# Performance work log

Measured on AMD Instinct MI355X. Metric: run time of the kernel, lower is better.

Reference implementation:

```python
import jax, jax.numpy as jnp
import numpy as np

B, T, C = 4, 1024, 512
H, HD = 8, 64
NE, K = 8, 2
FF = 4 * C


def setup_inputs() -> dict:
    key = jax.random.key(0)
    ks = jax.random.split(key, 16)
    s = 0.02
    return {
        "x": jax.random.normal(ks[0], (B, T, C), jnp.float32),
        "ln1_g": jnp.ones((C,), jnp.float32),
        "ln1_b": jnp.zeros((C,), jnp.float32),
        "ln2_g": jnp.ones((C,), jnp.float32),
        "ln2_b": jnp.zeros((C,), jnp.float32),
        "Wq": jax.random.normal(ks[1], (H, C, HD), jnp.float32) * s,
        "Wk": jax.random.normal(ks[2], (H, C, HD), jnp.float32) * s,
        "Wv": jax.random.normal(ks[3], (H, C, HD), jnp.float32) * s,
        "Wp": jax.random.normal(ks[4], (H * HD, C), jnp.float32) * s,
        "bp": jnp.zeros((C,), jnp.float32),
        "Wr": jax.random.normal(ks[5], (C, NE), jnp.float32) * s,
        "br": jnp.zeros((NE,), jnp.float32),
        "W1": jax.random.normal(ks[6], (NE, C, FF), jnp.float32) * s,
        "b1": jnp.zeros((NE, FF), jnp.float32),
        "W2": jax.random.normal(ks[7], (NE, FF, C), jnp.float32) * s,
        "b2": jnp.zeros((NE, C), jnp.float32),
    }


def _ln(x, g, b, eps=1e-5):
    mu = jnp.mean(x, axis=-1, keepdims=True)
    var = jnp.var(x, axis=-1, keepdims=True)
    return (x - mu) * jax.lax.rsqrt(var + eps) * g + b


def reference(x, ln1_g, ln1_b, ln2_g, ln2_b, Wq, Wk, Wv, Wp, bp, Wr, br, W1, b1, W2, b2):
    # --- multi-head causal attention (all heads stacked) ---
    h = _ln(x, ln1_g, ln1_b)
    q = jnp.einsum("btc,hcd->bhtd", h, Wq)
    k = jnp.einsum("btc,hcd->bhtd", h, Wk)
    v = jnp.einsum("btc,hcd->bhtd", h, Wv)
    wei = jnp.einsum("bhtd,bhsd->bhts", q, k) / np.sqrt(HD).astype(np.float32)
    causal = jnp.tril(jnp.ones((T, T), bool))
    wei = jnp.where(causal, wei, -jnp.inf)
    wei = jax.nn.softmax(wei, axis=-1)
    attn = jnp.einsum("bhts,bhsd->bhtd", wei, v)  # [B,H,T,HD]
    attn = attn.transpose(0, 2, 1, 3).reshape(B, T, H * HD)
    x2 = x + attn @ Wp + bp

    # --- SparseMoE: dense all-experts compute, masked top-k combine ---
    h2 = _ln(x2, ln2_g, ln2_b)
    scores = h2 @ Wr + br  # [B,T,NE]
    topk_scores, indices = jax.lax.top_k(scores, K)
    # scatter top-k scores into zeros (rest stays 0), then softmax over experts
    mask = jnp.sum(jax.nn.one_hot(indices, NE, dtype=scores.dtype) * topk_scores[..., None], axis=-2)
    router = jax.nn.softmax(mask, axis=-1)  # [B,T,NE]
    hid = jax.nn.relu(jnp.einsum("btc,ecf->btef", h2, W1) + b1)  # [B,T,NE,FF]
    eo = jnp.einsum("btef,efc->btec", hid, W2) + b2  # [B,T,NE,C]
    moe = jnp.einsum("bte,btec->btc", router, eo)
    return x2 + moe
```

## Files before the change

kernel.cpp:

```cpp
#include <hip/hip_runtime.h>


typedef unsigned short u16;
typedef __attribute__((ext_vector_type(8))) short s16x8;
typedef __attribute__((ext_vector_type(4))) float f32x4;

__device__ __forceinline__ u16 f2bf(float f) {
  union { float f; unsigned u; } v; v.f = f;
  unsigned r = v.u + 0x7fffu + ((v.u >> 16) & 1u);
  return (u16)(r >> 16);
}
__device__ __forceinline__ float bf2f(u16 h) {
  union { unsigned u; float f; } v; v.u = ((unsigned)h) << 16;
  return v.f;
}

#define GLDS16(g, s) __builtin_amdgcn_global_load_lds( \
    (const __attribute__((address_space(1))) void*)(g), \
    (__attribute__((address_space(3))) void*)(s), 16, 0, 0)

#define MFMA16(a, b, c) __builtin_amdgcn_mfma_f32_16x16x32_bf16((a), (b), (c), 0, 0, 0)

__global__ __launch_bounds__(256) void transpose_k(
    const float* __restrict__ in, u16* __restrict__ out,
    int R, int C, long long ibs, long long obs, float scale)
{
  __shared__ float tile[32][33];
  in  += (long long)blockIdx.z * ibs;
  out += (long long)blockIdx.z * obs;
  const int c0 = blockIdx.x * 32, r0 = blockIdx.y * 32;
  const int tx = threadIdx.x, ty = threadIdx.y;
  #pragma unroll
  for (int i = 0; i < 4; ++i)
    tile[ty + i*8][tx] = in[(size_t)(r0 + ty + i*8) * C + c0 + tx];
  __syncthreads();
  #pragma unroll
  for (int i = 0; i < 4; ++i)
    out[(size_t)(c0 + ty + i*8) * R + r0 + tx] = f2bf(tile[tx][ty + i*8] * scale);
}

__global__ __launch_bounds__(256) void transqkv_k(
    const float* __restrict__ Wq, const float* __restrict__ Wk,
    const float* __restrict__ Wv, u16* __restrict__ out)
{
  __shared__ float tile[32][33];
  const int z = blockIdx.z, which = z >> 3, head = z & 7;
  const float* in = (which == 0 ? Wq : (which == 1 ? Wk : Wv)) + (size_t)head * 512 * 64;
  u16* o = out + (size_t)which * 512 * 512 + (size_t)head * 64 * 512;
  const float scale = (which == 0) ? 0.125f : 1.f;
  const int c0 = blockIdx.x * 32, r0 = blockIdx.y * 32;
  const int tx = threadIdx.x, ty = threadIdx.y;
  #pragma unroll
  for (int i = 0; i < 4; ++i)
    tile[ty + i*8][tx] = in[(size_t)(r0 + ty + i*8) * 64 + c0 + tx];
  __syncthreads();
  #pragma unroll
  for (int i = 0; i < 4; ++i)
    o[(size_t)(c0 + ty + i*8) * 512 + r0 + tx] = f2bf(tile[tx][ty + i*8] * scale);
}

__global__ __launch_bounds__(256) void vtrans_k(
    const u16* __restrict__ qkv, u16* __restrict__ vt)
{
  __shared__ u16 tile[32][33];
  const int bh = blockIdx.z, b = bh >> 3, h = bh & 7;
  const int t0 = blockIdx.x * 32, d0 = blockIdx.y * 32;
  const int tx = threadIdx.x, ty = threadIdx.y;
  #pragma unroll
  for (int i = 0; i < 4; ++i)
    tile[ty + i*8][tx] = qkv[(size_t)(b*1024 + t0 + ty + i*8) * 1536 + 1024 + h*64 + d0 + tx];
  __syncthreads();
  #pragma unroll
  for (int i = 0; i < 4; ++i)
    vt[(size_t)bh*65536 + (size_t)(d0 + ty + i*8) * 1024 + t0 + tx] = tile[tx][ty + i*8];
}

__global__ __launch_bounds__(256) void ln_k(
    const float* __restrict__ x, const float* __restrict__ g,
    const float* __restrict__ b, u16* __restrict__ o)
{
  const int row = blockIdx.x, t = threadIdx.x;
  const float* xr = x + (size_t)row * 512;
  const float a0 = xr[t], a1 = xr[t + 256];
  float s = a0 + a1, ss = a0*a0 + a1*a1;
  #pragma unroll
  for (int off = 1; off < 64; off <<= 1) {
    s  += __shfl_xor(s, off);
    ss += __shfl_xor(ss, off);
  }
  __shared__ float rs[4], rq[4];
  const int w = t >> 6;
  if ((t & 63) == 0) { rs[w] = s; rq[w] = ss; }
  __syncthreads();
  s  = rs[0] + rs[1] + rs[2] + rs[3];
  ss = rq[0] + rq[1] + rq[2] + rq[3];
  const float mu = s * (1.f/512.f);
  const float var = ss * (1.f/512.f) - mu*mu;
  const float rstd = rsqrtf(var + 1e-5f);
  o[(size_t)row*512 + t]       = f2bf((a0 - mu) * rstd * g[t]     + b[t]);
  o[(size_t)row*512 + t + 256] = f2bf((a1 - mu) * rstd * g[t+256] + b[t+256]);
}

template<int BN, int EPI>
__global__ __launch_bounds__(256) void gemm2p(
    const u16* __restrict__ A, const u16* __restrict__ Bt,
    int M, int N, int K, int lda, int ldb,
    u16* __restrict__ obf, float* __restrict__ oa,
    const float* __restrict__ bias, const float* __restrict__ extra, int e0)
{
  constexpr int NB = BN / 32;
  constexpr int SB = BN / 32;
  __shared__ u16 Asm[2][128*64];
  __shared__ u16 Bsm[2][BN*64];
  const int t = threadIdx.x, l = t & 63;
  const int wid = t >> 6, wr = wid >> 1, wc = wid & 1;
  const int lrow = l & 15, lhi = l >> 4;
  const int m0 = blockIdx.x * 128, n0 = blockIdx.y * BN;

  const f32x4 z4 = {0.f, 0.f, 0.f, 0.f};
  f32x4 acc[4][NB];
  #pragma unroll
  for (int i = 0; i < 4; ++i)
    #pragma unroll
    for (int j = 0; j < NB; ++j) acc[i][j] = z4;

  const u16* ga = A  + (size_t)(m0 + (t >> 3)) * lda + (t & 7) * 8;
  const u16* gb = Bt + (size_t)(n0 + (t >> 3)) * ldb + (t & 7) * 8;

#define STG2(buf, k0) do { \
    _Pragma("unroll") \
    for (int i = 0; i < 4; ++i) \
      GLDS16(ga + (size_t)(i*32)*lda + (k0), (char*)Asm[buf] + i*4096 + t*16); \
    _Pragma("unroll") \
    for (int i = 0; i < SB; ++i) \
      GLDS16(gb + (size_t)(i*32)*ldb + (k0), (char*)Bsm[buf] + i*4096 + t*16); \
  } while (0)

  const int NT = K >> 6;
  STG2(0, 0);
  for (int tt = 0; tt < NT; ++tt) {
    if (tt + 1 < NT) {
      STG2((tt + 1) & 1, (tt + 1) * 64);
      if constexpr (BN == 128) asm volatile("s_waitcnt vmcnt(8)" ::: "memory");
      else                     asm volatile("s_waitcnt vmcnt(6)" ::: "memory");
    } else {
      asm volatile("s_waitcnt vmcnt(0)" ::: "memory");
    }
    __builtin_amdgcn_sched_barrier(0);
    __builtin_amdgcn_s_barrier();
    const u16* As = Asm[tt & 1];
    const u16* Bs = Bsm[tt & 1];
    #pragma unroll
    for (int kh = 0; kh < 2; ++kh) {
      s16x8 af[4], bfr[NB];
      #pragma unroll
      for (int i = 0; i < 4; ++i)
        af[i]  = *(const s16x8*)(As + (wr*64 + i*16 + lrow)*64 + kh*32 + lhi*8);
      #pragma unroll
      for (int j = 0; j < NB; ++j)
        bfr[j] = *(const s16x8*)(Bs + (wc*(BN/2) + j*16 + lrow)*64 + kh*32 + lhi*8);
      #pragma unroll
      for (int i = 0; i < 4; ++i)
        #pragma unroll
        for (int j = 0; j < NB; ++j)
          acc[i][j] = MFMA16(af[i], bfr[j], acc[i][j]);
    }
    __builtin_amdgcn_s_barrier();
    __builtin_amdgcn_sched_barrier(0);
  }
#undef STG2

  #pragma unroll
  for (int i = 0; i < 4; ++i) {
    const int rbase = m0 + wr*64 + i*16 + lhi*4;
    #pragma unroll
    for (int j = 0; j < NB; ++j) {
      const int col = n0 + wc*(BN/2) + j*16 + lrow;
      #pragma unroll
      for (int rr = 0; rr < 4; ++rr) {
        const int row = rbase + rr;
        const float v = acc[i][j][rr];
        if (EPI == 0) {
          obf[(size_t)row*N + col] = f2bf(v);
        } else if (EPI == 1) {
          const float r = extra[(size_t)row*8 + e0 + (col >> 11)];
          obf[(size_t)row*N + col] = f2bf(fmaxf(v + bias[col], 0.f) * r);
        } else {
          oa[(size_t)row*N + col] = v + bias[col] + extra[(size_t)row*N + col];
        }
      }
    }
  }
}

template<int NKT, int EPI>
__global__ __launch_bounds__(512, 2) void gemm8p(
    const u16* __restrict__ A, const u16* __restrict__ Bt,
    int lda, int ldb,
    u16* __restrict__ obf,
    const float* __restrict__ bias, const float* __restrict__ rout)
{
  __shared__ u16 Lds[2][2][256*64];
  const int t = threadIdx.x, l = t & 63;
  const int wid = t >> 6, wm = wid >> 2, wn = wid & 3;
  const int lrow = l & 15, lhi = l >> 4;

  int m0, n0, zz = 0;
  {
    const int bid = blockIdx.x;
    const int r = bid & 7, k = bid >> 3;
    if (EPI == 1) { m0 = (k >> 3) * 256; n0 = (r * 8 + (k & 7)) * 256; }
    else { zz = r + (k >> 3) * 8; m0 = ((k & 7) >> 1) * 256; n0 = (k & 1) * 256; }
  }
  const u16* Ab = A  + (size_t)m0 * lda + (EPI == 4 ? zz * 512 : 0);
  const u16* Bb = Bt + (size_t)n0 * ldb + (EPI == 4 ? zz * 512 : 0);

  const int tr = t >> 3;
  const int sc = ((t & 7) ^ (tr & 7)) * 8;

#define STG(bf, kt, hx) do { \
    const int X_ = (hx) >> 1, h_ = (hx) & 1; \
    const u16* s_ = X_ ? Bb : Ab; \
    const int ld_ = X_ ? ldb : lda; \
    char* d_ = (char*)&Lds[bf][X_][0] + h_*16384 + t*16; \
    GLDS16(s_ + (size_t)(h_*128 + tr) * ld_ + (kt)*64 + sc, d_); \
    GLDS16(s_ + (size_t)(h_*128 + 64 + tr) * ld_ + (kt)*64 + sc, d_ + 8192); \
  } while (0)

#define RD(Ls, row, kb) (*(const s16x8*)((const char*)(Ls) + (row)*128 + ((kb) ^ (((row)&7)<<4))))

  f32x4 acc[8][4];
  const f32x4 z4 = {0.f, 0.f, 0.f, 0.f};
  #pragma unroll
  for (int i = 0; i < 8; ++i)
    #pragma unroll
    for (int j = 0; j < 4; ++j) acc[i][j] = z4;

  #pragma unroll
  for (int kt = 0; kt < 2; ++kt)
    #pragma unroll
    for (int hx = 0; hx < 4; ++hx) STG(kt & 1, kt, hx);
  asm volatile("s_waitcnt vmcnt(8)" ::: "memory");
  __builtin_amdgcn_sched_barrier(0);
  __builtin_amdgcn_s_barrier();

  s16x8 frA[2][4], frB[2][2];
  #pragma unroll
  for (int X = 0; X < NKT; ++X) {
    const u16* As = &Lds[X & 1][0][0];
    const u16* Bs = &Lds[X & 1][1][0];
    #pragma unroll
    for (int q = 0; q < 4; ++q) {
      const int mh = q >> 1, nh = q & 1;
      if (nh == 0) {
        #pragma unroll
        for (int kk = 0; kk < 2; ++kk)
          #pragma unroll
          for (int mf = 0; mf < 4; ++mf) {
            const int row = wm*128 + (mh*4 + mf)*16 + lrow;
            frA[kk][mf] = RD(As, row, kk*64 + lhi*16);
          }
      }
      #pragma unroll
      for (int kk = 0; kk < 2; ++kk)
        #pragma unroll
        for (int nf = 0; nf < 2; ++nf) {
          const int row = wn*64 + (nh*2 + nf)*16 + lrow;
          frB[kk][nf] = RD(Bs, row, kk*64 + lhi*16);
        }
      {
        const int P = 4*X + q;
        if (P >= 3) {
          const int kts = ((P - 3) >> 2) + 2, hh = (P - 3) & 3;
          if (kts < NKT) STG(kts & 1, kts, hh);
        }
      }
      __builtin_amdgcn_s_barrier();
      asm volatile("s_waitcnt lgkmcnt(0)" ::: "memory");
      __builtin_amdgcn_sched_barrier(0);
      __builtin_amdgcn_s_setprio(1);
      #pragma unroll
      for (int kk = 0; kk < 2; ++kk)
        #pragma unroll
        for (int mf = 0; mf < 4; ++mf)
          #pragma unroll
          for (int nf = 0; nf < 2; ++nf)
            acc[mh*4 + mf][nh*2 + nf] =
                MFMA16(frA[kk][mf], frB[kk][nf], acc[mh*4 + mf][nh*2 + nf]);
      __builtin_amdgcn_s_setprio(0);
      if (q == 3 && X + 1 < NKT) {
        if (X + 2 < NKT) asm volatile("s_waitcnt vmcnt(2)" ::: "memory");
        else             asm volatile("s_waitcnt vmcnt(0)" ::: "memory");
        __builtin_amdgcn_sched_barrier(0);
      }
      __builtin_amdgcn_s_barrier();
    }
  }
#undef STG
#undef RD

  u16* outp = (EPI == 4) ? obf + (size_t)zz * 1024 * 512 : obf;
  #pragma unroll
  for (int mf = 0; mf < 8; ++mf) {
    const int rbase = m0 + wm*128 + mf*16 + lhi*4;
    #pragma unroll
    for (int nf = 0; nf < 4; ++nf) {
      const int col = n0 + wn*64 + nf*16 + lrow;
      #pragma unroll
      for (int rr = 0; rr < 4; ++rr) {
        const int row = rbase + rr;
        const float v = acc[mf][nf][rr];
        if (EPI == 1) {
          const float r = rout[(size_t)row*8 + (col >> 11)];
          outp[(size_t)row*16384 + col] = f2bf(fmaxf(v + bias[col], 0.f) * r);
        } else {
          outp[(size_t)row*512 + col] = f2bf(v);
        }
      }
    }
  }
}

__global__ __launch_bounds__(256) void combineQ_k(
    float* __restrict__ outq, const u16* __restrict__ P,
    const float* __restrict__ routq, const float* __restrict__ b2)
{
  const int row = blockIdx.x, t = threadIdx.x;
  const int c = t * 2;
  float r[8];
  #pragma unroll
  for (int e = 0; e < 8; ++e) r[e] = routq[(size_t)row*8 + e];
  float v0 = outq[(size_t)row*512 + c];
  float v1 = outq[(size_t)row*512 + c + 1];
  #pragma unroll
  for (int z = 0; z < 32; ++z) {
    const unsigned pv = *(const unsigned*)(P + (size_t)z*524288 + (size_t)row*512 + c);
    v0 += bf2f((u16)(pv & 0xffffu));
    v1 += bf2f((u16)(pv >> 16));
  }
  #pragma unroll
  for (int e = 0; e < 8; ++e) {
    v0 += r[e] * b2[(size_t)e*512 + c];
    v1 += r[e] * b2[(size_t)e*512 + c + 1];
  }
  outq[(size_t)row*512 + c]     = v0;
  outq[(size_t)row*512 + c + 1] = v1;
}

__global__ __launch_bounds__(256) void gemm2_k(
    const u16* __restrict__ hid, const u16* __restrict__ w2t,
    u16* __restrict__ P, int e0, int accum)
{
  __shared__ u16 Asm[128*64];
  __shared__ u16 Bsm[64*64];
  const int t = threadIdx.x;
  const int l = t & 63;
  const int wid = t >> 6, wr = wid >> 1, wc = wid & 1;
  const int lrow = l & 15, lhi = l >> 4;
  const int m0 = blockIdx.x * 128, n0 = blockIdx.y * 64, z = blockIdx.z;

  const u16* A  = hid + z * 2048;
  const u16* Bt = w2t + (size_t)(e0 + z) * 512 * 2048;
  u16* Pz = P + (size_t)z * 4096 * 512;

  const f32x4 z4 = {0.f, 0.f, 0.f, 0.f};
  f32x4 acc[4][2];
  #pragma unroll
  for (int i = 0; i < 4; ++i) { acc[i][0] = z4; acc[i][1] = z4; }

  const u16* ga = A  + (size_t)(m0 + (t >> 3)) * 4096 + (t & 7) * 8;
  const u16* gb = Bt + (size_t)(n0 + (t >> 3)) * 2048 + (t & 7) * 8;

  for (int k0 = 0; k0 < 2048; k0 += 64) {
    #pragma unroll
    for (int i = 0; i < 4; ++i)
      GLDS16(ga + (size_t)i*32*4096 + k0, (char*)Asm + i*4096 + t*16);
    #pragma unroll
    for (int i = 0; i < 2; ++i)
      GLDS16(gb + (size_t)i*32*2048 + k0, (char*)Bsm + i*4096 + t*16);
    __syncthreads();
    #pragma unroll
    for (int kh = 0; kh < 2; ++kh) {
      s16x8 af[4], bfr[2];
      #pragma unroll
      for (int i = 0; i < 4; ++i)
        af[i]  = *(const s16x8*)(Asm + (wr*64 + i*16 + lrow)*64 + kh*32 + lhi*8);
      #pragma unroll
      for (int j = 0; j < 2; ++j)
        bfr[j] = *(const s16x8*)(Bsm + (wc*32 + j*16 + lrow)*64 + kh*32 + lhi*8);
      #pragma unroll
      for (int i = 0; i < 4; ++i)
        #pragma unroll
        for (int j = 0; j < 2; ++j)
          acc[i][j] = MFMA16(af[i], bfr[j], acc[i][j]);
    }
    __syncthreads();
  }

  #pragma unroll
  for (int i = 0; i < 4; ++i) {
    const int rbase = m0 + wr*64 + i*16 + lhi*4;
    #pragma unroll
    for (int j = 0; j < 2; ++j) {
      const int col = n0 + wc*32 + j*16 + lrow;
      #pragma unroll
      for (int rr = 0; rr < 4; ++rr) {
        const size_t idx = (size_t)(rbase + rr) * 512 + col;
        const float old = accum ? bf2f(Pz[idx]) : 0.f;
        Pz[idx] = f2bf(old + acc[i][j][rr]);
      }
    }
  }
}

__global__ __launch_bounds__(256) void combineB_k(
    float* __restrict__ out, const u16* __restrict__ P,
    const float* __restrict__ rout, const float* __restrict__ b2)
{
  const int row = blockIdx.x, t = threadIdx.x;
  float r[8];
  #pragma unroll
  for (int e = 0; e < 8; ++e) r[e] = rout[(size_t)row*8 + e];
  #pragma unroll
  for (int cc = 0; cc < 2; ++cc) {
    const int c = t + cc*256;
    const size_t idx = (size_t)row*512 + c;
    float v = out[idx] + bf2f(P[idx]) + bf2f(P[(size_t)4096*512 + idx]);
    #pragma unroll
    for (int e = 0; e < 8; ++e) v += r[e] * b2[(size_t)e*512 + c];
    out[idx] = v;
  }
}

__global__ __launch_bounds__(256) void attn_k(
    const u16* __restrict__ qkv, const u16* __restrict__ vt, u16* __restrict__ o)
{
  const int bid = blockIdx.x;
  const int xcd = bid & 7, rr_ = bid >> 3;
  const int bh = (rr_ >> 4) * 8 + xcd;
  const int qb = rr_ & 15;
  const int b = bh >> 3, h = bh & 7;
  const int t = threadIdx.x, l = t & 63, w = t >> 6;
  const int lrow = l & 15, lhi = l >> 4;
  const int t0w = qb*64 + w*16;

  __shared__ u16 Ksm[2][64*64];
  __shared__ u16 Vsm[2][64*64];
  __shared__ u16 Psm[4][16][72];

  const u16* qrow = qkv + (size_t)(b*1024 + t0w + lrow) * 1536 + h*64 + lhi*8;
  s16x8 qf0 = *(const s16x8*)qrow;
  s16x8 qf1 = *(const s16x8*)(qrow + 32);

  const f32x4 z4 = {0.f,0.f,0.f,0.f};
  float m[4], sl[4];
  f32x4 oacc[4];
  #pragma unroll
  for (int i = 0; i < 4; ++i) { m[i] = -1e30f; sl[i] = 0.f; oacc[i] = z4; }

  const int trow = t >> 3;
  const int csw = ((t & 7) ^ (trow & 7)) * 8;
  const u16* gk = qkv + (size_t)(b*1024 + trow) * 1536 + 512 + h*64 + csw;
  const u16* gv = vt + (size_t)bh*65536 + (size_t)trow*1024 + csw;
  const int nt = qb + 1;

#define ASTAGE(buf, s0) do { \
    _Pragma("unroll") \
    for (int i = 0; i < 2; ++i) { \
      GLDS16(gk + (size_t)((s0) + i*32) * 1536, (char*)Ksm[buf] + i*4096 + t*16); \
      GLDS16(gv + (s0) + (size_t)(i*32)*1024,   (char*)Vsm[buf] + i*4096 + t*16); \
    } } while (0)

  ASTAGE(0, 0);
  for (int kv = 0; kv < nt; ++kv) {
    const int s0 = kv * 64;
    if (kv + 1 < nt) {
      ASTAGE((kv + 1) & 1, s0 + 64);
      asm volatile("s_waitcnt vmcnt(4)" ::: "memory");
    } else {
      asm volatile("s_waitcnt vmcnt(0)" ::: "memory");
    }
    __builtin_amdgcn_s_barrier();
    __builtin_amdgcn_sched_barrier(0);
    const u16* Ks = Ksm[kv & 1];
    const u16* Vs = Vsm[kv & 1];

    f32x4 sacc[4] = {z4, z4, z4, z4};
    #pragma unroll
    for (int n = 0; n < 4; ++n) {
      const int r = n*16 + lrow;
      s16x8 kf0 = *(const s16x8*)((const char*)Ks + r*128 + ((lhi*16) ^ ((r & 7) << 4)));
      s16x8 kf1 = *(const s16x8*)((const char*)Ks + r*128 + ((64 + lhi*16) ^ ((r & 7) << 4)));
      sacc[n] = MFMA16(qf0, kf0, sacc[n]);
      sacc[n] = MFMA16(qf1, kf1, sacc[n]);
    }
    if (s0 + 63 > t0w) {
      #pragma unroll
      for (int n = 0; n < 4; ++n)
        #pragma unroll
        for (int rr = 0; rr < 4; ++rr)
          if (s0 + n*16 + lrow > t0w + lhi*4 + rr) sacc[n][rr] = -1e30f;
    }
    float pm[4];
    #pragma unroll
    for (int rr = 0; rr < 4; ++rr)
      pm[rr] = fmaxf(fmaxf(sacc[0][rr], sacc[1][rr]), fmaxf(sacc[2][rr], sacc[3][rr]));
    #pragma unroll
    for (int rr = 0; rr < 4; ++rr) {
      pm[rr] = fmaxf(pm[rr], __shfl_xor(pm[rr], 1));
      pm[rr] = fmaxf(pm[rr], __shfl_xor(pm[rr], 2));
      pm[rr] = fmaxf(pm[rr], __shfl_xor(pm[rr], 4));
      pm[rr] = fmaxf(pm[rr], __shfl_xor(pm[rr], 8));
    }
    float p[4][4], ps[4], scv[4];
    #pragma unroll
    for (int rr = 0; rr < 4; ++rr) {
      const float mn = fmaxf(m[rr], pm[rr]);
      scv[rr] = __expf(m[rr] - mn);
      m[rr] = mn;
      ps[rr] = 0.f;
      #pragma unroll
      for (int n = 0; n < 4; ++n) {
        p[n][rr] = __expf(sacc[n][rr] - mn);
        ps[rr] += p[n][rr];
      }
    }
    #pragma unroll
    for (int rr = 0; rr < 4; ++rr) {
      ps[rr] += __shfl_xor(ps[rr], 1);
      ps[rr] += __shfl_xor(ps[rr], 2);
      ps[rr] += __shfl_xor(ps[rr], 4);
      ps[rr] += __shfl_xor(ps[rr], 8);
      sl[rr] = sl[rr] * scv[rr] + ps[rr];
    }
    #pragma unroll
    for (int ct = 0; ct < 4; ++ct) {
      f32x4 t4 = oacc[ct];
      #pragma unroll
      for (int rr = 0; rr < 4; ++rr) t4[rr] *= scv[rr];
      oacc[ct] = t4;
    }
    #pragma unroll
    for (int n = 0; n < 4; ++n)
      #pragma unroll
      for (int rr = 0; rr < 4; ++rr)
        Psm[w][lhi*4 + rr][n*16 + lrow] = f2bf(p[n][rr]);
    asm volatile("s_waitcnt lgkmcnt(0)" ::: "memory");
    __builtin_amdgcn_sched_barrier(0);
    s16x8 pa0 = *(const s16x8*)&Psm[w][lrow][lhi*8];
    s16x8 pa1 = *(const s16x8*)&Psm[w][lrow][32 + lhi*8];
    #pragma unroll
    for (int ct = 0; ct < 4; ++ct) {
      const int r = ct*16 + lrow;
      s16x8 vb0 = *(const s16x8*)((const char*)Vs + r*128 + ((lhi*16) ^ ((r & 7) << 4)));
      s16x8 vb1 = *(const s16x8*)((const char*)Vs + r*128 + ((64 + lhi*16) ^ ((r & 7) << 4)));
      oacc[ct] = MFMA16(pa0, vb0, oacc[ct]);
      oacc[ct] = MFMA16(pa1, vb1, oacc[ct]);
    }
    __builtin_amdgcn_s_barrier();
    __builtin_amdgcn_sched_barrier(0);
  }
#undef ASTAGE
  #pragma unroll
  for (int ct = 0; ct < 4; ++ct)
    #pragma unroll
    for (int rr = 0; rr < 4; ++rr) {
      const int row = b*1024 + t0w + lhi*4 + rr;
      o[(size_t)row*512 + h*64 + ct*16 + lrow] = f2bf(oacc[ct][rr] / sl[rr]);
    }
}

__global__ __launch_bounds__(256) void router_k(
    const float* __restrict__ x2, const float* __restrict__ g,
    const float* __restrict__ b, const float* __restrict__ Wr,
    const float* __restrict__ br, float* __restrict__ rt,
    u16* __restrict__ h2o)
{
  const int l = threadIdx.x & 63, w = threadIdx.x >> 6;
  const int tkn = blockIdx.x * 4 + w;
  const float* xr = x2 + (size_t)tkn * 512;
  float v[8];
  float s = 0.f, ss = 0.f;
  #pragma unroll
  for (int i = 0; i < 8; ++i) {
    v[i] = xr[l*8 + i];
    s += v[i]; ss += v[i]*v[i];
  }
  #pragma unroll
  for (int off = 1; off < 64; off <<= 1) {
    s  += __shfl_xor(s, off);
    ss += __shfl_xor(ss, off);
  }
  const float mu = s * (1.f/512.f);
  const float var = ss * (1.f/512.f) - mu*mu;
  const float rstd = rsqrtf(var + 1e-5f);
  float acc[8];
  #pragma unroll
  for (int e = 0; e < 8; ++e) acc[e] = 0.f;
  s16x8 hw;
  #pragma unroll
  for (int i = 0; i < 8; ++i) {
    const int c = l*8 + i;
    const float hv = (v[i] - mu) * rstd * g[c] + b[c];
    hw[i] = (short)f2bf(hv);
    const float* wrow = Wr + (size_t)c * 8;
    #pragma unroll
    for (int e = 0; e < 8; ++e) acc[e] += hv * wrow[e];
  }
  *(s16x8*)(h2o + (size_t)tkn*512 + l*8) = hw;
  #pragma unroll
  for (int e = 0; e < 8; ++e) {
    #pragma unroll
    for (int off = 1; off < 64; off <<= 1) acc[e] += __shfl_xor(acc[e], off);
    acc[e] += br[e];
  }
  int e1 = 0;
  #pragma unroll
  for (int e = 1; e < 8; ++e) if (acc[e] > acc[e1]) e1 = e;
  int e2 = (e1 == 0) ? 1 : 0;
  #pragma unroll
  for (int e = 0; e < 8; ++e) if (e != e1 && acc[e] > acc[e2]) e2 = e;
  const float mx = fmaxf(acc[e1], 0.f);
  float Z = 0.f;
  #pragma unroll
  for (int e = 0; e < 8; ++e) {
    const float mv = (e == e1 || e == e2) ? acc[e] : 0.f;
    Z += __expf(mv - mx);
  }
  if (l < 8) {
    const float mv = (l == e1 || l == e2) ? acc[l] : 0.f;
    rt[(size_t)tkn * 8 + l] = __expf(mv - mx) / Z;
  }
}

extern "C" void kernel_launch(void* const* d_in, const int* in_sizes, int n_in,
                              void* d_out, int out_size, void* d_ws, size_t ws_size,
                              hipStream_t stream) {
  const float* x    = (const float*)d_in[0];
  const float* ln1g = (const float*)d_in[1];
  const float* ln1b = (const float*)d_in[2];
  const float* ln2g = (const float*)d_in[3];
  const float* ln2b = (const float*)d_in[4];
  const float* Wq   = (const float*)d_in[5];
  const float* Wk   = (const float*)d_in[6];
  const float* Wv   = (const float*)d_in[7];
  const float* Wp   = (const float*)d_in[8];
  const float* bp   = (const float*)d_in[9];
  const float* Wr   = (const float*)d_in[10];
  const float* br   = (const float*)d_in[11];
  const float* W1   = (const float*)d_in[12];
  const float* b1   = (const float*)d_in[13];
  const float* W2   = (const float*)d_in[14];
  const float* b2   = (const float*)d_in[15];
  float* out = (float*)d_out;

  const int pathN = (ws_size >= (size_t)104988672) ? 1 : 0;

  char* ws = (char*)d_ws;
  size_t off = 0;
  auto alloc = [&](size_t bytes) -> char* {
    char* p = ws + off;
    off += (bytes + 255) & ~(size_t)255;
    return p;
  };
  u16* w1_t = (u16*)alloc((size_t)8*2048*512*2);
  u16* w2f  = (u16*)alloc((size_t)8*512*2048*2);
  u16* h2b  = (u16*)alloc((size_t)4096*512*2);
  float* rout = (float*)alloc((size_t)4096*8*4);
  u16* hidq = (u16*)alloc((size_t)4096*4096*2);
  u16* Ppl  = (u16*)alloc(pathN ? (size_t)32*1024*512*2
                                : (size_t)2*4096*512*2);
  u16* wqkv_t = (u16*)hidq;
  u16* wp_t   = (u16*)((char*)hidq + 1572864);
  u16* hb     = (u16*)((char*)hidq + 2097152);
  u16* attnb  = (u16*)((char*)hidq + 6291456);
  u16* qkvb   = (u16*)((char*)hidq + 10485760);
  u16* vtb    = (u16*)((char*)hidq + 23068672);

  const dim3 tb(32, 8);
  transqkv_k<<<dim3(2,16,24), tb, 0, stream>>>(Wq, Wk, Wv, wqkv_t);
  transpose_k<<<dim3(16,16,1), tb, 0, stream>>>(Wp, wp_t, 512, 512, 0, 0, 1.f);
  transpose_k<<<dim3(64,16,8), tb, 0, stream>>>(W1, w1_t, 512, 2048, (long long)512*2048, (long long)2048*512, 1.f);
  if (pathN)
    transpose_k<<<dim3(16,512,1), tb, 0, stream>>>(W2, w2f, 16384, 512, 0, 0, 1.f);
  else
    transpose_k<<<dim3(16,64,8), tb, 0, stream>>>(W2, w2f, 2048, 512, (long long)2048*512, (long long)512*2048, 1.f);

  ln_k<<<4096, 256, 0, stream>>>(x, ln1g, ln1b, hb);
  gemm2p<128,0><<<dim3(32,12), 256, 0, stream>>>(hb, wqkv_t, 4096, 1536, 512, 512, 512,
                                                 qkvb, nullptr, nullptr, nullptr, 0);
  vtrans_k<<<dim3(32,2,32), tb, 0, stream>>>(qkvb, vtb);
  attn_k<<<512, 256, 0, stream>>>(qkvb, vtb, attnb);
  gemm2p<64,2><<<dim3(32,8), 256, 0, stream>>>(attnb, wp_t, 4096, 512, 512, 512, 512,
                                               nullptr, out, bp, x, 0);
  router_k<<<1024, 256, 0, stream>>>(out, ln2g, ln2b, Wr, br, rout, h2b);

  if (pathN) {
    for (int q = 0; q < 4; ++q) {
      gemm8p<8,1><<<256, 512, 0, stream>>>(h2b + (size_t)q*1024*512, w1_t, 512, 512,
                                           hidq, b1, rout + (size_t)q*8192);
      gemm8p<8,4><<<256, 512, 0, stream>>>(hidq, w2f, 16384, 16384,
                                           Ppl, nullptr, nullptr);
      combineQ_k<<<1024, 256, 0, stream>>>(out + (size_t)q*1024*512, Ppl,
                                           rout + (size_t)q*8192, b2);
    }
  } else {
    for (int p = 0; p < 4; ++p) {
      const int e0 = 2*p;
      gemm2p<128,1><<<dim3(32,32), 256, 0, stream>>>(h2b, w1_t + (size_t)e0*2048*512,
                                                     4096, 4096, 512, 512, 512,
                                                     hidq, nullptr, b1 + (size_t)e0*2048, rout, e0);
      gemm2_k<<<dim3(32,8,2), 256, 0, stream>>>(hidq, w2f, Ppl, e0, p > 0 ? 1 : 0);
    }
    combineB_k<<<4096, 256, 0, stream>>>(out, Ppl, rout, b2);
  }
}
```

Measured before the change: 314.7 us.

## Halve MoE chunk count, pair causal attention blocks, fuse Wp transpose

Adds a larger-workspace MoE path that processes tokens in two halves of 2048 rows instead of four quarters. The second GEMM uses 16 split-K chunks of 1024, and a templated combine kernel reduces them. Attention blocks now each process a short and a long causal query tile (qb and 15-qb), which balances work and halves the grid. The Wp transpose is folded into the QKV transpose launch. Fewer launches and better load balance are traded for a larger workspace and fewer, heavier attention blocks.

```diff
diff --git a/kernel.cpp b/kernel.cpp
--- a/kernel.cpp
+++ b/kernel.cpp
@@ -41,22 +41,37 @@
 
 __global__ __launch_bounds__(256) void transqkv_k(
     const float* __restrict__ Wq, const float* __restrict__ Wk,
-    const float* __restrict__ Wv, u16* __restrict__ out)
+    const float* __restrict__ Wv, const float* __restrict__ Wp,
+    u16* __restrict__ oqkv, u16* __restrict__ owp)
 {
   __shared__ float tile[32][33];
-  const int z = blockIdx.z, which = z >> 3, head = z & 7;
-  const float* in = (which == 0 ? Wq : (which == 1 ? Wk : Wv)) + (size_t)head * 512 * 64;
-  u16* o = out + (size_t)which * 512 * 512 + (size_t)head * 64 * 512;
-  const float scale = (which == 0) ? 0.125f : 1.f;
-  const int c0 = blockIdx.x * 32, r0 = blockIdx.y * 32;
+  const int z = blockIdx.z;
   const int tx = threadIdx.x, ty = threadIdx.y;
-  #pragma unroll
-  for (int i = 0; i < 4; ++i)
-    tile[ty + i*8][tx] = in[(size_t)(r0 + ty + i*8) * 64 + c0 + tx];
-  __syncthreads();
-  #pragma unroll
-  for (int i = 0; i < 4; ++i)
-    o[(size_t)(c0 + ty + i*8) * 512 + r0 + tx] = f2bf(tile[tx][ty + i*8] * scale);
+  if (z < 24) {
+    const int which = z >> 3, head = z & 7;
+    const float* in = (which == 0 ? Wq : (which == 1 ? Wk : Wv)) + (size_t)head * 512 * 64;
+    u16* o = oqkv + (size_t)which * 512 * 512 + (size_t)head * 64 * 512;
+    const float scale = (which == 0) ? 0.125f : 1.f;
+    const int c0 = blockIdx.x * 32, r0 = blockIdx.y * 32;
+    #pragma unroll
+    for (int i = 0; i < 4; ++i)
+      tile[ty + i*8][tx] = in[(size_t)(r0 + ty + i*8) * 64 + c0 + tx];
+    __syncthreads();
+    #pragma unroll
+    for (int i = 0; i < 4; ++i)
+      o[(size_t)(c0 + ty + i*8) * 512 + r0 + tx] = f2bf(tile[tx][ty + i*8] * scale);
+  } else {
+    const int zz = z - 24;
+    const int c0 = (zz * 2 + blockIdx.x) * 32;
+    const int r0 = blockIdx.y * 32;
+    #pragma unroll
+    for (int i = 0; i < 4; ++i)
+      tile[ty + i*8][tx] = Wp[(size_t)(r0 + ty + i*8) * 512 + c0 + tx];
+    __syncthreads();
+    #pragma unroll
+    for (int i = 0; i < 4; ++i)
+      owp[(size_t)(c0 + ty + i*8) * 512 + r0 + tx] = f2bf(tile[tx][ty + i*8]);
+  }
 }
 
 __global__ __launch_bounds__(256) void vtrans_k(
@@ -208,12 +223,23 @@
   int m0, n0, zz = 0;
   {
     const int bid = blockIdx.x;
-    const int r = bid & 7, k = bid >> 3;
-    if (EPI == 1) { m0 = (k >> 3) * 256; n0 = (r * 8 + (k & 7)) * 256; }
-    else { zz = r + (k >> 3) * 8; m0 = ((k & 7) >> 1) * 256; n0 = (k & 1) * 256; }
-  }
-  const u16* Ab = A  + (size_t)m0 * lda + (EPI == 4 ? zz * 512 : 0);
-  const u16* Bb = Bt + (size_t)n0 * ldb + (EPI == 4 ? zz * 512 : 0);
+    if (EPI == 1) {
+      const int r = bid & 7, k = bid >> 3;
+      m0 = (k >> 3) * 256; n0 = (r * 8 + (k & 7)) * 256;
+    } else if (EPI == 2) {
+      const int nb = (bid & 7) * 64 + (bid >> 3);
+      m0 = (nb >> 6) * 256; n0 = (nb & 63) * 256;
+    } else if (EPI == 4) {
+      const int r = bid & 7, k = bid >> 3;
+      zz = r + (k >> 3) * 8; m0 = ((k & 7) >> 1) * 256; n0 = (k & 1) * 256;
+    } else {
+      zz = bid & 15; const int mn = bid >> 4;
+      m0 = (mn >> 1) * 256; n0 = (mn & 1) * 256;
+    }
+  }
+  constexpr int KCH = (EPI == 4) ? 512 : 1024;
+  const u16* Ab = A  + (size_t)m0 * lda + ((EPI == 4 || EPI == 5) ? zz * KCH : 0);
+  const u16* Bb = Bt + (size_t)n0 * ldb + ((EPI == 4 || EPI == 5) ? zz * KCH : 0);
 
   const int tr = t >> 3;
   const int sc = ((t & 7) ^ (tr & 7)) * 8;
@@ -299,7 +325,8 @@
 #undef STG
 #undef RD
 
-  u16* outp = (EPI == 4) ? obf + (size_t)zz * 1024 * 512 : obf;
+  constexpr size_t PSTRIDE = (EPI == 4) ? (size_t)1024*512 : (size_t)2048*512;
+  u16* outp = (EPI == 4 || EPI == 5) ? obf + (size_t)zz * PSTRIDE : obf;
   #pragma unroll
   for (int mf = 0; mf < 8; ++mf) {
     const int rbase = m0 + wm*128 + mf*16 + lhi*4;
@@ -310,7 +337,7 @@
       for (int rr = 0; rr < 4; ++rr) {
         const int row = rbase + rr;
         const float v = acc[mf][nf][rr];
-        if (EPI == 1) {
+        if (EPI == 1 || EPI == 2) {
           const float r = rout[(size_t)row*8 + (col >> 11)];
           outp[(size_t)row*16384 + col] = f2bf(fmaxf(v + bias[col], 0.f) * r);
         } else {
@@ -321,8 +348,9 @@
   }
 }
 
-__global__ __launch_bounds__(256) void combineQ_k(
-    float* __restrict__ outq, const u16* __restrict__ P,
+template<int Z>
+__global__ __launch_bounds__(256) void combineZ_k(
+    float* __restrict__ outq, const u16* __restrict__ P, size_t pstride,
     const float* __restrict__ routq, const float* __restrict__ b2)
 {
   const int row = blockIdx.x, t = threadIdx.x;
@@ -333,8 +361,8 @@
   float v0 = outq[(size_t)row*512 + c];
   float v1 = outq[(size_t)row*512 + c + 1];
   #pragma unroll
-  for (int z = 0; z < 32; ++z) {
-    const unsigned pv = *(const unsigned*)(P + (size_t)z*524288 + (size_t)row*512 + c);
+  for (int z = 0; z < Z; ++z) {
+    const unsigned pv = *(const unsigned*)(P + (size_t)z*pstride + (size_t)row*512 + c);
     v0 += bf2f((u16)(pv & 0xffffu));
     v1 += bf2f((u16)(pv >> 16));
   }
@@ -437,32 +465,21 @@
 {
   const int bid = blockIdx.x;
   const int xcd = bid & 7, rr_ = bid >> 3;
-  const int bh = (rr_ >> 4) * 8 + xcd;
-  const int qb = rr_ & 15;
+  const int bh = (rr_ >> 3) * 8 + xcd;
+  const int qp = rr_ & 7;
   const int b = bh >> 3, h = bh & 7;
   const int t = threadIdx.x, l = t & 63, w = t >> 6;
   const int lrow = l & 15, lhi = l >> 4;
-  const int t0w = qb*64 + w*16;
 
   __shared__ u16 Ksm[2][64*64];
   __shared__ u16 Vsm[2][64*64];
   __shared__ u16 Psm[4][16][72];
-
-  const u16* qrow = qkv + (size_t)(b*1024 + t0w + lrow) * 1536 + h*64 + lhi*8;
-  s16x8 qf0 = *(const s16x8*)qrow;
-  s16x8 qf1 = *(const s16x8*)(qrow + 32);
-
-  const f32x4 z4 = {0.f,0.f,0.f,0.f};
-  float m[4], sl[4];
-  f32x4 oacc[4];
-  #pragma unroll
-  for (int i = 0; i < 4; ++i) { m[i] = -1e30f; sl[i] = 0.f; oacc[i] = z4; }
 
   const int trow = t >> 3;
   const int csw = ((t & 7) ^ (trow & 7)) * 8;
   const u16* gk = qkv + (size_t)(b*1024 + trow) * 1536 + 512 + h*64 + csw;
   const u16* gv = vt + (size_t)bh*65536 + (size_t)trow*1024 + csw;
-  const int nt = qb + 1;
+  const f32x4 z4 = {0.f,0.f,0.f,0.f};
 
 #define ASTAGE(buf, s0) do { \
     _Pragma("unroll") \
@@ -471,103 +488,117 @@
       GLDS16(gv + (s0) + (size_t)(i*32)*1024,   (char*)Vsm[buf] + i*4096 + t*16); \
     } } while (0)
 
-  ASTAGE(0, 0);
-  for (int kv = 0; kv < nt; ++kv) {
-    const int s0 = kv * 64;
-    if (kv + 1 < nt) {
-      ASTAGE((kv + 1) & 1, s0 + 64);
-      asm volatile("s_waitcnt vmcnt(4)" ::: "memory");
-    } else {
-      asm volatile("s_waitcnt vmcnt(0)" ::: "memory");
-    }
-    __builtin_amdgcn_s_barrier();
-    __builtin_amdgcn_sched_barrier(0);
-    const u16* Ks = Ksm[kv & 1];
-    const u16* Vs = Vsm[kv & 1];
-
-    f32x4 sacc[4] = {z4, z4, z4, z4};
-    #pragma unroll
-    for (int n = 0; n < 4; ++n) {
-      const int r = n*16 + lrow;
-      s16x8 kf0 = *(const s16x8*)((const char*)Ks + r*128 + ((lhi*16) ^ ((r & 7) << 4)));
-      s16x8 kf1 = *(const s16x8*)((const char*)Ks + r*128 + ((64 + lhi*16) ^ ((r & 7) << 4)));
-      sacc[n] = MFMA16(qf0, kf0, sacc[n]);
-      sacc[n] = MFMA16(qf1, kf1, sacc[n]);
-    }
-    if (s0 + 63 > t0w) {
+  for (int pass = 0; pass < 2; ++pass) {
+    const int qb = pass ? (15 - qp) : qp;
+    const int t0w = qb*64 + w*16;
+    const u16* qrow = qkv + (size_t)(b*1024 + t0w + lrow) * 1536 + h*64 + lhi*8;
+    s16x8 qf0 = *(const s16x8*)qrow;
+    s16x8 qf1 = *(const s16x8*)(qrow + 32);
+
+    float m[4], sl[4];
+    f32x4 oacc[4];
+    #pragma unroll
+    for (int i = 0; i < 4; ++i) { m[i] = -1e30f; sl[i] = 0.f; oacc[i] = z4; }
+
+    const int nt = qb + 1;
+    ASTAGE(0, 0);
+    for (int kv = 0; kv < nt; ++kv) {
+      const int s0 = kv * 64;
+      if (kv + 1 < nt) {
+        ASTAGE((kv + 1) & 1, s0 + 64);
+        asm volatile("s_waitcnt vmcnt(4)" ::: "memory");
+      } else {
+        asm volatile("s_waitcnt vmcnt(0)" ::: "memory");
+      }
+      __builtin_amdgcn_s_barrier();
+      __builtin_amdgcn_sched_barrier(0);
+      const u16* Ks = Ksm[kv & 1];
+      const u16* Vs = Vsm[kv & 1];
+
+      f32x4 sacc[4] = {z4, z4, z4, z4};
+      #pragma unroll
+      for (int n = 0; n < 4; ++n) {
+        const int r = n*16 + lrow;
+        s16x8 kf0 = *(const s16x8*)((const char*)Ks + r*128 + ((lhi*16) ^ ((r & 7) << 4)));
+        s16x8 kf1 = *(const s16x8*)((const char*)Ks + r*128 + ((64 + lhi*16) ^ ((r & 7) << 4)));
+        sacc[n] = MFMA16(qf0, kf0, sacc[n]);
+        sacc[n] = MFMA16(qf1, kf1, sacc[n]);
+      }
+      if (s0 + 63 > t0w) {
+        #pragma unroll
+        for (int n = 0; n < 4; ++n)
+          #pragma unroll
+          for (int rr = 0; rr < 4; ++rr)
+            if (s0 + n*16 + lrow > t0w + lhi*4 + rr) sacc[n][rr] = -1e30f;
+      }
+      float pm[4];
+      #pragma unroll
+      for (int rr = 0; rr < 4; ++rr)
+        pm[rr] = fmaxf(fmaxf(sacc[0][rr], sacc[1][rr]), fmaxf(sacc[2][rr], sacc[3][rr]));
+      #pragma unroll
+      for (int rr = 0; rr < 4; ++rr) {
+        pm[rr] = fmaxf(pm[rr], __shfl_xor(pm[rr], 1));
+        pm[rr] = fmaxf(pm[rr], __shfl_xor(pm[rr], 2));
+        pm[rr] = fmaxf(pm[rr], __shfl_xor(pm[rr], 4));
+        pm[rr] = fmaxf(pm[rr], __shfl_xor(pm[rr], 8));
+      }
+      float p[4][4], ps[4], scv[4];
+      #pragma unroll
+      for (int rr = 0; rr < 4; ++rr) {
+        const float mn = fmaxf(m[rr], pm[rr]);
+        scv[rr] = __expf(m[rr] - mn);
+        m[rr] = mn;
+        ps[rr] = 0.f;
+        #pragma unroll
+        for (int n = 0; n < 4; ++n) {
+          p[n][rr] = __expf(sacc[n][rr] - mn);
+          ps[rr] += p[n][rr];
+        }
+      }
+      #pragma unroll
+      for (int rr = 0; rr < 4; ++rr) {
+        ps[rr] += __shfl_xor(ps[rr], 1);
+        ps[rr] += __shfl_xor(ps[rr], 2);
+        ps[rr] += __shfl_xor(ps[rr], 4);
+        ps[rr] += __shfl_xor(ps[rr], 8);
+        sl[rr] = sl[rr] * scv[rr] + ps[rr];
+      }
+      #pragma unroll
+      for (int ct = 0; ct < 4; ++ct) {
+        f32x4 t4 = oacc[ct];
+        #pragma unroll
+        for (int rr = 0; rr < 4; ++rr) t4[rr] *= scv[rr];
+        oacc[ct] = t4;
+      }
       #pragma unroll
       for (int n = 0; n < 4; ++n)
         #pragma unroll
         for (int rr = 0; rr < 4; ++rr)
-          if (s0 + n*16 + lrow > t0w + lhi*4 + rr) sacc[n][rr] = -1e30f;
-    }
-    float pm[4];
-    #pragma unroll
-    for (int rr = 0; rr < 4; ++rr)
-      pm[rr] = fmaxf(fmaxf(sacc[0][rr], sacc[1][rr]), fmaxf(sacc[2][rr], sacc[3][rr]));
-    #pragma unroll
-    for (int rr = 0; rr < 4; ++rr) {
-      pm[rr] = fmaxf(pm[rr], __shfl_xor(pm[rr], 1));
-      pm[rr] = fmaxf(pm[rr], __shfl_xor(pm[rr], 2));
-      pm[rr] = fmaxf(pm[rr], __shfl_xor(pm[rr], 4));
-      pm[rr] = fmaxf(pm[rr], __shfl_xor(pm[rr], 8));
-    }
-    float p[4][4], ps[4], scv[4];
-    #pragma unroll
-    for (int rr = 0; rr < 4; ++rr) {
-      const float mn = fmaxf(m[rr], pm[rr]);
-      scv[rr] = __expf(m[rr] - mn);
-      m[rr] = mn;
-      ps[rr] = 0.f;
-      #pragma unroll
-      for (int n = 0; n < 4; ++n) {
-        p[n][rr] = __expf(sacc[n][rr] - mn);
-        ps[rr] += p[n][rr];
-      }
-    }
-    #pragma unroll
-    for (int rr = 0; rr < 4; ++rr) {
-      ps[rr] += __shfl_xor(ps[rr], 1);
-      ps[rr] += __shfl_xor(ps[rr], 2);
-      ps[rr] += __shfl_xor(ps[rr], 4);
-      ps[rr] += __shfl_xor(ps[rr], 8);
-      sl[rr] = sl[rr] * scv[rr] + ps[rr];
-    }
-    #pragma unroll
-    for (int ct = 0; ct < 4; ++ct) {
-      f32x4 t4 = oacc[ct];
-      #pragma unroll
-      for (int rr = 0; rr < 4; ++rr) t4[rr] *= scv[rr];
-      oacc[ct] = t4;
-    }
-    #pragma unroll
-    for (int n = 0; n < 4; ++n)
-      #pragma unroll
-      for (int rr = 0; rr < 4; ++rr)
-        Psm[w][lhi*4 + rr][n*16 + lrow] = f2bf(p[n][rr]);
-    asm volatile("s_waitcnt lgkmcnt(0)" ::: "memory");
-    __builtin_amdgcn_sched_barrier(0);
-    s16x8 pa0 = *(const s16x8*)&Psm[w][lrow][lhi*8];
-    s16x8 pa1 = *(const s16x8*)&Psm[w][lrow][32 + lhi*8];
-    #pragma unroll
-    for (int ct = 0; ct < 4; ++ct) {
-      const int r = ct*16 + lrow;
-      s16x8 vb0 = *(const s16x8*)((const char*)Vs + r*128 + ((lhi*16) ^ ((r & 7) << 4)));
-      s16x8 vb1 = *(const s16x8*)((const char*)Vs + r*128 + ((64 + lhi*16) ^ ((r & 7) << 4)));
-      oacc[ct] = MFMA16(pa0, vb0, oacc[ct]);
-      oacc[ct] = MFMA16(pa1, vb1, oacc[ct]);
-    }
-    __builtin_amdgcn_s_barrier();
-    __builtin_amdgcn_sched_barrier(0);
+          Psm[w][lhi*4 + rr][n*16 + lrow] = f2bf(p[n][rr]);
+      asm volatile("s_waitcnt lgkmcnt(0)" ::: "memory");
+      __builtin_amdgcn_sched_barrier(0);
+      s16x8 pa0 = *(const s16x8*)&Psm[w][lrow][lhi*8];
+      s16x8 pa1 = *(const s16x8*)&Psm[w][lrow][32 + lhi*8];
+      #pragma unroll
+      for (int ct = 0; ct < 4; ++ct) {
+        const int r = ct*16 + lrow;
+        s16x8 vb0 = *(const s16x8*)((const char*)Vs + r*128 + ((lhi*16) ^ ((r & 7) << 4)));
+        s16x8 vb1 = *(const s16x8*)((const char*)Vs + r*128 + ((64 + lhi*16) ^ ((r & 7) << 4)));
+        oacc[ct] = MFMA16(pa0, vb0, oacc[ct]);
+        oacc[ct] = MFMA16(pa1, vb1, oacc[ct]);
+      }
+      __builtin_amdgcn_s_barrier();
+      __builtin_amdgcn_sched_barrier(0);
+    }
+    #pragma unroll
+    for (int ct = 0; ct < 4; ++ct)
+      #pragma unroll
+      for (int rr = 0; rr < 4; ++rr) {
+        const int row = b*1024 + t0w + lhi*4 + rr;
+        o[(size_t)row*512 + h*64 + ct*16 + lrow] = f2bf(oacc[ct][rr] / sl[rr]);
+      }
   }
 #undef ASTAGE
-  #pragma unroll
-  for (int ct = 0; ct < 4; ++ct)
-    #pragma unroll
-    for (int rr = 0; rr < 4; ++rr) {
-      const int row = b*1024 + t0w + lhi*4 + rr;
-      o[(size_t)row*512 + h*64 + ct*16 + lrow] = f2bf(oacc[ct][rr] / sl[rr]);
-    }
 }
 
 __global__ __launch_bounds__(256) void router_k(
@@ -654,6 +685,7 @@
   const float* b2   = (const float*)d_in[15];
   float* out = (float*)d_out;
 
+  const int pathH = (ws_size >= (size_t)138543104) ? 1 : 0;
   const int pathN = (ws_size >= (size_t)104988672) ? 1 : 0;
 
   char* ws = (char*)d_ws;
@@ -667,9 +699,9 @@
   u16* w2f  = (u16*)alloc((size_t)8*512*2048*2);
   u16* h2b  = (u16*)alloc((size_t)4096*512*2);
   float* rout = (float*)alloc((size_t)4096*8*4);
-  u16* hidq = (u16*)alloc((size_t)4096*4096*2);
-  u16* Ppl  = (u16*)alloc(pathN ? (size_t)32*1024*512*2
-                                : (size_t)2*4096*512*2);
+  u16* hidq = (u16*)alloc(pathH ? (size_t)2048*16384*2 : (size_t)4096*4096*2);
+  u16* Ppl  = (u16*)alloc(pathH ? (size_t)16*2048*512*2
+                                : (pathN ? (size_t)32*1024*512*2 : (size_t)2*4096*512*2));
   u16* wqkv_t = (u16*)hidq;
   u16* wp_t   = (u16*)((char*)hidq + 1572864);
   u16* hb     = (u16*)((char*)hidq + 2097152);
@@ -678,8 +710,7 @@
   u16* vtb    = (u16*)((char*)hidq + 23068672);
 
   const dim3 tb(32, 8);
-  transqkv_k<<<dim3(2,16,24), tb, 0, stream>>>(Wq, Wk, Wv, wqkv_t);
-  transpose_k<<<dim3(16,16,1), tb, 0, stream>>>(Wp, wp_t, 512, 512, 0, 0, 1.f);
+  transqkv_k<<<dim3(2,16,32), tb, 0, stream>>>(Wq, Wk, Wv, Wp, wqkv_t, wp_t);
   transpose_k<<<dim3(64,16,8), tb, 0, stream>>>(W1, w1_t, 512, 2048, (long long)512*2048, (long long)2048*512, 1.f);
   if (pathN)
     transpose_k<<<dim3(16,512,1), tb, 0, stream>>>(W2, w2f, 16384, 512, 0, 0, 1.f);
@@ -690,19 +721,30 @@
   gemm2p<128,0><<<dim3(32,12), 256, 0, stream>>>(hb, wqkv_t, 4096, 1536, 512, 512, 512,
                                                  qkvb, nullptr, nullptr, nullptr, 0);
   vtrans_k<<<dim3(32,2,32), tb, 0, stream>>>(qkvb, vtb);
-  attn_k<<<512, 256, 0, stream>>>(qkvb, vtb, attnb);
+  attn_k<<<256, 256, 0, stream>>>(qkvb, vtb, attnb);
   gemm2p<64,2><<<dim3(32,8), 256, 0, stream>>>(attnb, wp_t, 4096, 512, 512, 512, 512,
                                                nullptr, out, bp, x, 0);
   router_k<<<1024, 256, 0, stream>>>(out, ln2g, ln2b, Wr, br, rout, h2b);
 
-  if (pathN) {
+  if (pathH) {
+    for (int h = 0; h < 2; ++h) {
+      gemm8p<8,2><<<512, 512, 0, stream>>>(h2b + (size_t)h*2048*512, w1_t, 512, 512,
+                                           hidq, b1, rout + (size_t)h*16384);
+      gemm8p<16,5><<<256, 512, 0, stream>>>(hidq, w2f, 16384, 16384,
+                                            Ppl, nullptr, nullptr);
+      combineZ_k<16><<<2048, 256, 0, stream>>>(out + (size_t)h*2048*512, Ppl,
+                                               (size_t)2048*512,
+                                               rout + (size_t)h*16384, b2);
+    }
+  } else if (pathN) {
     for (int q = 0; q < 4; ++q) {
       gemm8p<8,1><<<256, 512, 0, stream>>>(h2b + (size_t)q*1024*512, w1_t, 512, 512,
                                            hidq, b1, rout + (size_t)q*8192);
       gemm8p<8,4><<<256, 512, 0, stream>>>(hidq, w2f, 16384, 16384,
                                            Ppl, nullptr, nullptr);
-      combineQ_k<<<1024, 256, 0, stream>>>(out + (size_t)q*1024*512, Ppl,
-                                           rout + (size_t)q*8192, b2);
+      combineZ_k<32><<<1024, 256, 0, stream>>>(out + (size_t)q*1024*512, Ppl,
+                                               (size_t)1024*512,
+                                               rout + (size_t)q*8192, b2);
     }
   } else {
     for (int p = 0; p < 4; ++p) {
```

New measurement: 279.1 us. 1.13x faster.
